# Optimization experiments

Measured on AMD Instinct MI355X. Metric: run time of the kernel, lower is better.

Reference implementation:

```python
import jax, jax.numpy as jnp
import numpy as np

TOPK_RATIOS = (0.67, 0.75, 0.8)


def setup_inputs() -> dict:
    key = jax.random.key(0)
    k0, k1, k2 = jax.random.split(key, 3)
    B, L, S, H, E, D = 4, 2048, 2048, 8, 64, 64
    queries = jax.random.normal(k0, (B, L, H, E), dtype=jnp.float32)
    keys = jax.random.normal(k1, (B, S, H, E), dtype=jnp.float32)
    values = jax.random.normal(k2, (B, S, H, D), dtype=jnp.float32)
    attn_weights = jnp.ones((len(TOPK_RATIOS),), dtype=jnp.float32)  # nn.Parameter(ones)
    attn_mask = jnp.zeros((1,), dtype=bool)  # unused by the module
    return {"queries": queries, "keys": keys, "values": values,
            "attn_weights": attn_weights, "attn_mask": attn_mask}


def reference(queries, keys, values, attn_weights, attn_mask):
    # queries: [B,L,H,E], keys: [B,S,H,E], values: [B,S,H,D]
    B, L, H, E = queries.shape
    S = keys.shape[1]
    scale = 1.0 / np.sqrt(E)  # self.scale is None -> 1/sqrt(E)
    scores = jnp.einsum('blhe,bshe->bhls', queries, keys) * scale  # [B,H,L,S]
    out = jnp.zeros(queries.shape[:3] + (values.shape[-1],), dtype=scores.dtype)
    for i, ratio in enumerate(TOPK_RATIOS):
        k = int(S * ratio)
        topv = jax.lax.top_k(scores, k)[0]            # sorted descending
        kth = topv[..., -1:]                           # k-th largest per row
        # mask==0 -> -inf, then softmax over S (ties at threshold are measure-zero)
        masked = jnp.where(scores >= kth, scores, -jnp.inf)
        attn = jax.nn.softmax(masked, axis=-1)         # dropout = identity (eval)
        out = out + jnp.einsum('bhls,bshd->blhd', attn, values) * attn_weights[i]
    return out
```

## Files before the change

kernel.cpp:

```cpp
#include <hip/hip_runtime.h>
#include <hip/hip_fp16.h>

typedef _Float16 f16x8 __attribute__((ext_vector_type(8)));
typedef float f32x4 __attribute__((ext_vector_type(4)));

#define KSEL0 1372u
#define KSEL1 1536u
#define KSEL2 1638u
#define WSC 16.0f
#define CSH 8.0f

__device__ __forceinline__ unsigned ou16_of(unsigned hb) {
  return hb ^ ((hb & 0x8000u) ? 0xFFFFu : 0x8000u);
}
__device__ __forceinline__ unsigned ou16_inv(unsigned ou) {
  return (ou & 0x8000u) ? (ou ^ 0x8000u) : (ou ^ 0xFFFFu);
}
__device__ __forceinline__ unsigned pk2(float a, float b) {
  auto h = __builtin_amdgcn_cvt_pkrtz(a, b);
  return __builtin_bit_cast(unsigned, h);
}
__device__ __forceinline__ unsigned shflx(unsigned v, int m) {
  return (unsigned)__shfl_xor((int)v, m, 64);
}
__device__ __forceinline__ float h2f(unsigned bits16) {
  return __half2float(__ushort_as_half((unsigned short)bits16));
}

__device__ __forceinline__ unsigned sel_digit_s(const unsigned* histw, unsigned k,
                                                int lane, int shift) {
  uint4 hr = ((const uint4*)histw)[lane];
  unsigned hx = (hr.x >> shift) & 0xFFFFu;
  unsigned hy = (hr.y >> shift) & 0xFFFFu;
  unsigned hz = (hr.z >> shift) & 0xFFFFu;
  unsigned hw_ = (hr.w >> shift) & 0xFFFFu;
  unsigned s4 = hx + hy + hz + hw_;
  unsigned p = s4;
  #pragma unroll
  for (int off = 1; off < 64; off <<= 1) {
    int sl = lane + off;
    unsigned t = (unsigned)__shfl((int)p, sl < 64 ? sl : lane, 64);
    p += (sl < 64) ? t : 0u;
  }
  unsigned a3 = p - s4;
  unsigned a2 = a3 + hw_;
  unsigned a1 = a2 + hz;
  unsigned a0 = a1 + hy;
  int d = -1; unsigned nk = 0;
  if (a3 < k && a3 + hw_ >= k)      { d = 4*lane+3; nk = k - a3; }
  else if (a2 < k && a2 + hz >= k)  { d = 4*lane+2; nk = k - a2; }
  else if (a1 < k && a1 + hy >= k)  { d = 4*lane+1; nk = k - a1; }
  else if (a0 < k && a0 + hx >= k)  { d = 4*lane+0; nk = k - a0; }
  unsigned long long mb = __ballot(d >= 0);
  int src = __ffsll(mb) - 1;
  unsigned pack = ((unsigned)d << 16) | nk;
  return (unsigned)__shfl((int)pack, src, 64);
}

extern "C" __global__ __launch_bounds__(256)
void prep_k(const float* __restrict__ K, unsigned short* __restrict__ Kh) {
  int idx = blockIdx.x * 256 + threadIdx.x;
  int ec = idx & 7;
  int s  = (idx >> 3) & 2047;
  int bh = idx >> 14;
  int b = bh >> 3, h = bh & 7;
  const float* src = K + (((size_t)b * 2048 + s) * 8 + h) * 64 + ec * 8;
  float4 a = *(const float4*)src;
  float4 c = *(const float4*)(src + 4);
  uint4 val = { pk2(a.x, a.y), pk2(a.z, a.w), pk2(c.x, c.y), pk2(c.z, c.w) };
  *(uint4*)(Kh + (size_t)idx * 8) = val;
}

extern "C" __global__ __launch_bounds__(256)
void prep_v(const float* __restrict__ V, unsigned short* __restrict__ Vt) {
  const int tid  = threadIdx.x;
  const int w    = tid >> 6;
  const int lane = tid & 63;
  const int u_   = lane >> 4;
  const int dq   = (lane >> 2) & 3;
  const int r_   = lane & 3;
  const unsigned selv = (lane & 1) ? 0x03020706u : 0x05040100u;

  int bh = blockIdx.x >> 4;
  int s0 = (blockIdx.x & 15) * 128;
  int b = bh >> 3, h = bh & 7;
  const float* Vb = V + ((size_t)b * 2048 * 8 + h) * 64;
  unsigned short* Vo = Vt + (size_t)bh * 64 * 2048;

  #pragma unroll
  for (int sp = 0; sp < 2; ++sp) {
    #pragma unroll
    for (int p = 0; p < 4; ++p) {
      int sl = w * 32 + sp * 16 + u_ * 4;
      int sg = s0 + sl + r_;
      int d0 = p * 16 + dq * 4;
      float4 f = *(const float4*)(Vb + (size_t)sg * 512 + d0);
      unsigned lo = pk2(f.x, f.y), hi = pk2(f.z, f.w);
      unsigned tlo = shflx(lo, 1), thi = shflx(hi, 1);
      lo = __builtin_amdgcn_perm(tlo, lo, selv);
      hi = __builtin_amdgcn_perm(thi, hi, selv);
      unsigned t2lo = shflx(lo, 2), t2hi = shflx(hi, 2);
      unsigned Aw = (lane & 2) ? t2hi : lo;
      unsigned Bw = (lane & 2) ? hi   : t2lo;
      int d = d0 + r_;
      uint2 wv = {Aw, Bw};
      *(uint2*)(Vo + (size_t)d * 2048 + s0 + sl) = wv;
    }
  }
}

extern "C" __global__ __launch_bounds__(512, 4)
void nma_kernel(const float* __restrict__ Q, const unsigned short* __restrict__ Kh,
                const unsigned short* __restrict__ Vt, const float* __restrict__ AW,
                float* __restrict__ Out)
{
  __shared__ __align__(16) char lds[81920];
  unsigned* work = (unsigned*)(lds + 65536);

  const int tid  = threadIdx.x;
  const int w    = tid >> 6;
  const int lane = tid & 63;
  const int g    = lane >> 4;
  const int lx   = lane & 15;

  int bid = blockIdx.x;
  int lb  = (bid & 7) * 512 + (bid >> 3);
  int bh  = lb >> 7;
  int b   = bh >> 3, hh = bh & 7;
  int l0  = (lb & 127) << 4;

  const float* Qb = Q + (((size_t)b * 2048 + l0) * 8 + hh) * 64;
  const unsigned short* Khb = Kh + (size_t)bh * 2048 * 64;
  const unsigned short* Vtb = Vt + (size_t)bh * 64 * 2048;

  {
    uint4 z4 = {0u,0u,0u,0u};
    uint4* p = (uint4*)work;
    p[tid] = z4;
    p[tid + 512] = z4;
  }

  union FU { f16x8 v; unsigned u[4]; };
  FU qa0, qa1;
  {
    const float* qp = Qb + (size_t)lx * 512 + g * 8;
    float4 a = *(const float4*)(qp);
    float4 c = *(const float4*)(qp + 4);
    qa0.u[0] = pk2(a.x*0.125f, a.y*0.125f); qa0.u[1] = pk2(a.z*0.125f, a.w*0.125f);
    qa0.u[2] = pk2(c.x*0.125f, c.y*0.125f); qa0.u[3] = pk2(c.z*0.125f, c.w*0.125f);
    a = *(const float4*)(qp + 32);
    c = *(const float4*)(qp + 36);
    qa1.u[0] = pk2(a.x*0.125f, a.y*0.125f); qa1.u[1] = pk2(a.z*0.125f, a.w*0.125f);
    qa1.u[2] = pk2(c.x*0.125f, c.y*0.125f); qa1.u[3] = pk2(c.z*0.125f, c.w*0.125f);
  }
  __syncthreads();

  const unsigned swl = ((unsigned)(lx & 7)) << 4;
  unsigned* hq = work + lx * 256;
  #pragma unroll 2
  for (int t = 0; t < 16; ++t) {
    int s0 = (t * 8 + w) * 16;
    const unsigned short* kp = Khb + (size_t)(s0 + lx) * 64 + g * 8;
    f16x8 kb0 = *(const f16x8*)(kp);
    f16x8 kb1 = *(const f16x8*)(kp + 32);
    f32x4 acc = {0.f, 0.f, 0.f, 0.f};
    acc = __builtin_amdgcn_mfma_f32_16x16x32_f16(kb0, qa0.v, acc, 0, 0, 0);
    acc = __builtin_amdgcn_mfma_f32_16x16x32_f16(kb1, qa1.v, acc, 0, 0, 0);
    unsigned u0 = pk2(acc[0], acc[1]);
    unsigned u1 = pk2(acc[2], acc[3]);
    uint2 wv = {u0, u1};
    *(uint2*)(lds + lx * 4096 + (((unsigned)(s0 * 2 + g * 8)) ^ swl)) = wv;
    atomicAdd(&hq[ou16_of(u0 & 0xFFFFu) >> 8], 1u);
    atomicAdd(&hq[ou16_of(u0 >> 16) >> 8], 1u);
    atomicAdd(&hq[ou16_of(u1 & 0xFFFFu) >> 8], 1u);
    atomicAdd(&hq[ou16_of(u1 >> 16) >> 8], 1u);
  }
  __syncthreads();

  const float aw0 = AW[0], aw1 = AW[1], aw2 = AW[2];

  unsigned d0a[2], d1a[2], d2a[2], k0a[2], k1a[2], k2a[2];
  #pragma unroll 2
  for (int rr = 0; rr < 2; ++rr) {
    int q = 2 * w + rr;
    const unsigned* hw1 = work + q * 256;
    unsigned p0 = sel_digit_s(hw1, KSEL0, lane, 0);
    unsigned p1 = sel_digit_s(hw1, KSEL1, lane, 0);
    unsigned p2 = sel_digit_s(hw1, KSEL2, lane, 0);
    d0a[rr] = p0 >> 16; k0a[rr] = p0 & 0xFFFFu;
    d1a[rr] = p1 >> 16; k1a[rr] = p1 & 0xFFFFu;
    d2a[rr] = p2 >> 16; k2a[rr] = p2 & 0xFFFFu;
  }

  unsigned* hw2 = work + w * 512;
  #pragma unroll 1
  for (int rr = 0; rr < 2; ++rr) {
    int q = 2 * w + rr;
    const unsigned swq = ((unsigned)(q & 7)) << 4;
    char* rowp = lds + q * 4096;
    for (int i = lane; i < 512; i += 64) hw2[i] = 0u;
    unsigned D0 = d0a[rr], D1 = d1a[rr], D2 = d2a[rr];

    unsigned ereg[16];
    #pragma unroll
    for (int it = 0; it < 4; ++it) {
      uint4 dv = *(const uint4*)(rowp + (((unsigned)(it * 1024 + lane * 16)) ^ swq));
      unsigned ws[4] = {dv.x, dv.y, dv.z, dv.w};
      #pragma unroll
      for (int p = 0; p < 4; ++p) {
        unsigned b0 = ws[p] & 0xFFFFu, b1 = ws[p] >> 16;
        unsigned o0 = ou16_of(b0), o1 = ou16_of(b1);
        unsigned hi0 = o0 >> 8, lo0 = o0 & 255u;
        unsigned hi1 = o1 >> 8, lo1 = o1 & 255u;
        unsigned add0 = (hi0 == D0 ? 1u : 0u) | (hi0 == D1 ? 0x10000u : 0u);
        unsigned add1 = (hi1 == D0 ? 1u : 0u) | (hi1 == D1 ? 0x10000u : 0u);
        if (add0) atomicAdd(&hw2[lo0], add0);
        if (hi0 == D2) atomicAdd(&hw2[256 + lo0], 1u);
        if (add1) atomicAdd(&hw2[lo1], add1);
        if (hi1 == D2) atomicAdd(&hw2[256 + lo1], 1u);
        float e0 = __expf(h2f(b0) - CSH);
        float e1 = __expf(h2f(b1) - CSH);
        ereg[it * 4 + p] = pk2(e0, e1);
      }
    }
    unsigned T1o = (D0 << 8) | (sel_digit_s(hw2,       k0a[rr], lane, 0)  >> 16);
    unsigned T2o = (D1 << 8) | (sel_digit_s(hw2,       k1a[rr], lane, 16) >> 16);
    unsigned T3o = (D2 << 8) | (sel_digit_s(hw2 + 256, k2a[rr], lane, 0)  >> 16);
    unsigned e1b = pk2(__expf(h2f(ou16_inv(T1o)) - CSH), 0.f) & 0xFFFFu;
    unsigned e2b = pk2(__expf(h2f(ou16_inv(T2o)) - CSH), 0.f) & 0xFFFFu;
    unsigned e3b = pk2(__expf(h2f(ou16_inv(T3o)) - CSH), 0.f) & 0xFFFFu;

    float zbA = 0.f, zbB = 0.f, zbC = 0.f;
    #pragma unroll
    for (int i = 0; i < 16; ++i) {
      unsigned uu = ereg[i];
      unsigned b0 = uu & 0xFFFFu, b1 = uu >> 16;
      float e0 = h2f(b0), e1 = h2f(b1);
      if (b0 >= e1b) zbA += e0; else if (b0 >= e2b) zbB += e0; else if (b0 >= e3b) zbC += e0;
      if (b1 >= e1b) zbA += e1; else if (b1 >= e2b) zbB += e1; else if (b1 >= e3b) zbC += e1;
    }
    #pragma unroll
    for (int off = 1; off < 64; off <<= 1) {
      zbA += __shfl_xor(zbA, off, 64);
      zbB += __shfl_xor(zbB, off, 64);
      zbC += __shfl_xor(zbC, off, 64);
    }
    float z1 = zbA, z2 = zbA + zbB, z3 = z2 + zbC;
    float A3 = aw2 / z3;
    float A2 = aw1 / z2 + A3;
    float A1 = aw0 / z1 + A2;
    unsigned A1b = pk2(A1 * WSC, 0.f) & 0xFFFFu;
    unsigned A2b = pk2(A2 * WSC, 0.f) & 0xFFFFu;
    unsigned A3b = pk2(A3 * WSC, 0.f) & 0xFFFFu;

    #pragma unroll
    for (int it = 0; it < 4; ++it) {
      unsigned no[4];
      #pragma unroll
      for (int p = 0; p < 4; ++p) {
        unsigned uu = ereg[it * 4 + p];
        unsigned b0 = uu & 0xFFFFu, b1 = uu >> 16;
        unsigned c0 = (b0 >= e1b) ? A1b : (b0 >= e2b) ? A2b : (b0 >= e3b) ? A3b : 0u;
        unsigned c1 = (b1 >= e1b) ? A1b : (b1 >= e2b) ? A2b : (b1 >= e3b) ? A3b : 0u;
        unsigned cw = c0 | (c1 << 16);
        __half2 prod = *(__half2*)&uu * *(__half2*)&cw;
        no[p] = *(unsigned*)&prod;
      }
      uint4 nv = {no[0], no[1], no[2], no[3]};
      *(uint4*)(rowp + (((unsigned)(it * 1024 + lane * 16)) ^ swq)) = nv;
    }
  }
  __syncthreads();

  f32x4 oacc = {0.f, 0.f, 0.f, 0.f};
  const int dt = (w >> 1) * 16;
  const int sh = w & 1;
  const unsigned short* vp = Vtb + (size_t)(dt + lx) * 2048 + sh * 1024 + g * 8;
  const char* bp = lds + lx * 4096;

  #pragma unroll 8
  for (int kc = 0; kc < 32; ++kc) {
    f16x8 av = *(const f16x8*)(vp + kc * 32);
    unsigned sb = (unsigned)((sh * 1024 + kc * 32 + g * 8) * 2);
    f16x8 bv = *(const f16x8*)(bp + (sb ^ swl));
    oacc = __builtin_amdgcn_mfma_f32_16x16x32_f16(av, bv, oacc, 0, 0, 0);
  }

  float* pbuf = (float*)work;
  *(f32x4*)(pbuf + w * 256 + lx * 16 + g * 4) = oacc;
  __syncthreads();
  if (w < 4) {
    const float* pa = pbuf + (2 * w) * 256 + lx * 16 + g * 4;
    float4 ra = *(const float4*)pa;
    float4 rb = *(const float4*)(pa + 256);
    float* op = Out + (((size_t)b * 2048 + l0 + lx) * 8 + hh) * 64 + w * 16 + g * 4;
    float4 ov = { (ra.x + rb.x) * (1.f/WSC), (ra.y + rb.y) * (1.f/WSC),
                  (ra.z + rb.z) * (1.f/WSC), (ra.w + rb.w) * (1.f/WSC) };
    *(float4*)op = ov;
  }
}

extern "C" void kernel_launch(void* const* d_in, const int* in_sizes, int n_in,
                              void* d_out, int out_size, void* d_ws, size_t ws_size,
                              hipStream_t stream) {
  (void)in_sizes; (void)n_in; (void)out_size; (void)ws_size;
  const float* Q  = (const float*)d_in[0];
  const float* K  = (const float*)d_in[1];
  const float* V  = (const float*)d_in[2];
  const float* AW = (const float*)d_in[3];
  unsigned short* Kh = (unsigned short*)d_ws;
  unsigned short* Vt = (unsigned short*)((char*)d_ws + 8388608);
  prep_k<<<dim3(2048), dim3(256), 0, stream>>>(K, Kh);
  prep_v<<<dim3(512),  dim3(256), 0, stream>>>(V, Vt);
  nma_kernel<<<dim3(4096), dim3(512), 0, stream>>>(Q, Kh, Vt, AW, (float*)d_out);
}
```

Before: 375.0 us.

## Merge prep kernels, rotate histogram bins, share prefix scans, prefetch V before barrier

Merges the K and V conversion kernels into one launch to save a kernel launch. Rotates each row's histogram bins by a per-row offset to spread LDS atomic bank conflicts, then unrotates the read by indexing with (lane+q)&63. Computes the 64-lane suffix scan once per histogram and shares it across the three threshold picks instead of rescanning each time. Prefetches the first V fragments before the final barrier and raises unroll factors. The rotation makes correctness depend on the unrotate indexing matching exactly.

```diff
diff --git a/kernel.cpp b/kernel.cpp
--- a/kernel.cpp
+++ b/kernel.cpp
@@ -27,14 +27,7 @@
   return __half2float(__ushort_as_half((unsigned short)bits16));
 }
 
-__device__ __forceinline__ unsigned sel_digit_s(const unsigned* histw, unsigned k,
-                                                int lane, int shift) {
-  uint4 hr = ((const uint4*)histw)[lane];
-  unsigned hx = (hr.x >> shift) & 0xFFFFu;
-  unsigned hy = (hr.y >> shift) & 0xFFFFu;
-  unsigned hz = (hr.z >> shift) & 0xFFFFu;
-  unsigned hw_ = (hr.w >> shift) & 0xFFFFu;
-  unsigned s4 = hx + hy + hz + hw_;
+__device__ __forceinline__ unsigned suffix64(unsigned s4, int lane) {
   unsigned p = s4;
   #pragma unroll
   for (int off = 1; off < 64; off <<= 1) {
@@ -42,7 +35,12 @@
     unsigned t = (unsigned)__shfl((int)p, sl < 64 ? sl : lane, 64);
     p += (sl < 64) ? t : 0u;
   }
-  unsigned a3 = p - s4;
+  return p;
+}
+__device__ __forceinline__ unsigned pick_digit(unsigned tail, unsigned hx, unsigned hy,
+                                               unsigned hz, unsigned hw_, unsigned k, int lane) {
+  unsigned s4 = hx + hy + hz + hw_;
+  unsigned a3 = tail - s4;
   unsigned a2 = a3 + hw_;
   unsigned a1 = a2 + hz;
   unsigned a0 = a1 + hy;
@@ -58,53 +56,54 @@
 }
 
 extern "C" __global__ __launch_bounds__(256)
-void prep_k(const float* __restrict__ K, unsigned short* __restrict__ Kh) {
-  int idx = blockIdx.x * 256 + threadIdx.x;
-  int ec = idx & 7;
-  int s  = (idx >> 3) & 2047;
-  int bh = idx >> 14;
-  int b = bh >> 3, h = bh & 7;
-  const float* src = K + (((size_t)b * 2048 + s) * 8 + h) * 64 + ec * 8;
-  float4 a = *(const float4*)src;
-  float4 c = *(const float4*)(src + 4);
-  uint4 val = { pk2(a.x, a.y), pk2(a.z, a.w), pk2(c.x, c.y), pk2(c.z, c.w) };
-  *(uint4*)(Kh + (size_t)idx * 8) = val;
-}
-
-extern "C" __global__ __launch_bounds__(256)
-void prep_v(const float* __restrict__ V, unsigned short* __restrict__ Vt) {
-  const int tid  = threadIdx.x;
-  const int w    = tid >> 6;
-  const int lane = tid & 63;
-  const int u_   = lane >> 4;
-  const int dq   = (lane >> 2) & 3;
-  const int r_   = lane & 3;
-  const unsigned selv = (lane & 1) ? 0x03020706u : 0x05040100u;
-
-  int bh = blockIdx.x >> 4;
-  int s0 = (blockIdx.x & 15) * 128;
-  int b = bh >> 3, h = bh & 7;
-  const float* Vb = V + ((size_t)b * 2048 * 8 + h) * 64;
-  unsigned short* Vo = Vt + (size_t)bh * 64 * 2048;
-
-  #pragma unroll
-  for (int sp = 0; sp < 2; ++sp) {
-    #pragma unroll
-    for (int p = 0; p < 4; ++p) {
-      int sl = w * 32 + sp * 16 + u_ * 4;
-      int sg = s0 + sl + r_;
-      int d0 = p * 16 + dq * 4;
-      float4 f = *(const float4*)(Vb + (size_t)sg * 512 + d0);
-      unsigned lo = pk2(f.x, f.y), hi = pk2(f.z, f.w);
-      unsigned tlo = shflx(lo, 1), thi = shflx(hi, 1);
-      lo = __builtin_amdgcn_perm(tlo, lo, selv);
-      hi = __builtin_amdgcn_perm(thi, hi, selv);
-      unsigned t2lo = shflx(lo, 2), t2hi = shflx(hi, 2);
-      unsigned Aw = (lane & 2) ? t2hi : lo;
-      unsigned Bw = (lane & 2) ? hi   : t2lo;
-      int d = d0 + r_;
-      uint2 wv = {Aw, Bw};
-      *(uint2*)(Vo + (size_t)d * 2048 + s0 + sl) = wv;
+void prep_kv(const float* __restrict__ K, const float* __restrict__ V,
+             unsigned short* __restrict__ Kh, unsigned short* __restrict__ Vt) {
+  if (blockIdx.x < 2048) {
+    int idx = blockIdx.x * 256 + threadIdx.x;
+    int ec = idx & 7;
+    int s  = (idx >> 3) & 2047;
+    int bh = idx >> 14;
+    int b = bh >> 3, h = bh & 7;
+    const float* src = K + (((size_t)b * 2048 + s) * 8 + h) * 64 + ec * 8;
+    float4 a = *(const float4*)src;
+    float4 c = *(const float4*)(src + 4);
+    uint4 val = { pk2(a.x, a.y), pk2(a.z, a.w), pk2(c.x, c.y), pk2(c.z, c.w) };
+    *(uint4*)(Kh + (size_t)idx * 8) = val;
+  } else {
+    const int bid  = blockIdx.x - 2048;
+    const int tid  = threadIdx.x;
+    const int w    = tid >> 6;
+    const int lane = tid & 63;
+    const int u_   = lane >> 4;
+    const int dq   = (lane >> 2) & 3;
+    const int r_   = lane & 3;
+    const unsigned selv = (lane & 1) ? 0x03020706u : 0x05040100u;
+
+    int bh = bid >> 4;
+    int s0 = (bid & 15) * 128;
+    int b = bh >> 3, h = bh & 7;
+    const float* Vb = V + ((size_t)b * 2048 * 8 + h) * 64;
+    unsigned short* Vo = Vt + (size_t)bh * 64 * 2048;
+
+    #pragma unroll
+    for (int sp = 0; sp < 2; ++sp) {
+      #pragma unroll
+      for (int p = 0; p < 4; ++p) {
+        int sl = w * 32 + sp * 16 + u_ * 4;
+        int sg = s0 + sl + r_;
+        int d0 = p * 16 + dq * 4;
+        float4 f = *(const float4*)(Vb + (size_t)sg * 512 + d0);
+        unsigned lo = pk2(f.x, f.y), hi = pk2(f.z, f.w);
+        unsigned tlo = shflx(lo, 1), thi = shflx(hi, 1);
+        lo = __builtin_amdgcn_perm(tlo, lo, selv);
+        hi = __builtin_amdgcn_perm(thi, hi, selv);
+        unsigned t2lo = shflx(lo, 2), t2hi = shflx(hi, 2);
+        unsigned Aw = (lane & 2) ? t2hi : lo;
+        unsigned Bw = (lane & 2) ? hi   : t2lo;
+        int d = d0 + r_;
+        uint2 wv = {Aw, Bw};
+        *(uint2*)(Vo + (size_t)d * 2048 + s0 + sl) = wv;
+      }
     }
   }
 }
@@ -156,8 +155,9 @@
   __syncthreads();
 
   const unsigned swl = ((unsigned)(lx & 7)) << 4;
+  const unsigned rot = ((unsigned)lx) << 2;
   unsigned* hq = work + lx * 256;
-  #pragma unroll 2
+  #pragma unroll 4
   for (int t = 0; t < 16; ++t) {
     int s0 = (t * 8 + w) * 16;
     const unsigned short* kp = Khb + (size_t)(s0 + lx) * 64 + g * 8;
@@ -170,10 +170,10 @@
     unsigned u1 = pk2(acc[2], acc[3]);
     uint2 wv = {u0, u1};
     *(uint2*)(lds + lx * 4096 + (((unsigned)(s0 * 2 + g * 8)) ^ swl)) = wv;
-    atomicAdd(&hq[ou16_of(u0 & 0xFFFFu) >> 8], 1u);
-    atomicAdd(&hq[ou16_of(u0 >> 16) >> 8], 1u);
-    atomicAdd(&hq[ou16_of(u1 & 0xFFFFu) >> 8], 1u);
-    atomicAdd(&hq[ou16_of(u1 >> 16) >> 8], 1u);
+    atomicAdd(&hq[((ou16_of(u0 & 0xFFFFu) >> 8) + rot) & 255u], 1u);
+    atomicAdd(&hq[((ou16_of(u0 >> 16) >> 8) + rot) & 255u], 1u);
+    atomicAdd(&hq[((ou16_of(u1 & 0xFFFFu) >> 8) + rot) & 255u], 1u);
+    atomicAdd(&hq[((ou16_of(u1 >> 16) >> 8) + rot) & 255u], 1u);
   }
   __syncthreads();
 
@@ -183,10 +183,11 @@
   #pragma unroll 2
   for (int rr = 0; rr < 2; ++rr) {
     int q = 2 * w + rr;
-    const unsigned* hw1 = work + q * 256;
-    unsigned p0 = sel_digit_s(hw1, KSEL0, lane, 0);
-    unsigned p1 = sel_digit_s(hw1, KSEL1, lane, 0);
-    unsigned p2 = sel_digit_s(hw1, KSEL2, lane, 0);
+    uint4 hb = ((const uint4*)(work + q * 256))[(lane + q) & 63];
+    unsigned tail = suffix64(hb.x + hb.y + hb.z + hb.w, lane);
+    unsigned p0 = pick_digit(tail, hb.x, hb.y, hb.z, hb.w, KSEL0, lane);
+    unsigned p1 = pick_digit(tail, hb.x, hb.y, hb.z, hb.w, KSEL1, lane);
+    unsigned p2 = pick_digit(tail, hb.x, hb.y, hb.z, hb.w, KSEL2, lane);
     d0a[rr] = p0 >> 16; k0a[rr] = p0 & 0xFFFFu;
     d1a[rr] = p1 >> 16; k1a[rr] = p1 & 0xFFFFu;
     d2a[rr] = p2 >> 16; k2a[rr] = p2 & 0xFFFFu;
@@ -223,9 +224,16 @@
         ereg[it * 4 + p] = pk2(e0, e1);
       }
     }
-    unsigned T1o = (D0 << 8) | (sel_digit_s(hw2,       k0a[rr], lane, 0)  >> 16);
-    unsigned T2o = (D1 << 8) | (sel_digit_s(hw2,       k1a[rr], lane, 16) >> 16);
-    unsigned T3o = (D2 << 8) | (sel_digit_s(hw2 + 256, k2a[rr], lane, 0)  >> 16);
+    uint4 pkv = ((const uint4*)hw2)[lane];
+    uint4 d2v = ((const uint4*)(hw2 + 256))[lane];
+    unsigned hx = pkv.x & 0xFFFFu, hy = pkv.y & 0xFFFFu, hz = pkv.z & 0xFFFFu, hw_ = pkv.w & 0xFFFFu;
+    unsigned t0 = suffix64(hx + hy + hz + hw_, lane);
+    unsigned T1o = (D0 << 8) | (pick_digit(t0, hx, hy, hz, hw_, k0a[rr], lane) >> 16);
+    hx = pkv.x >> 16; hy = pkv.y >> 16; hz = pkv.z >> 16; hw_ = pkv.w >> 16;
+    unsigned t1 = suffix64(hx + hy + hz + hw_, lane);
+    unsigned T2o = (D1 << 8) | (pick_digit(t1, hx, hy, hz, hw_, k1a[rr], lane) >> 16);
+    unsigned t2 = suffix64(d2v.x + d2v.y + d2v.z + d2v.w, lane);
+    unsigned T3o = (D2 << 8) | (pick_digit(t2, d2v.x, d2v.y, d2v.z, d2v.w, k2a[rr], lane) >> 16);
     unsigned e1b = pk2(__expf(h2f(ou16_inv(T1o)) - CSH), 0.f) & 0xFFFFu;
     unsigned e2b = pk2(__expf(h2f(ou16_inv(T2o)) - CSH), 0.f) & 0xFFFFu;
     unsigned e3b = pk2(__expf(h2f(ou16_inv(T3o)) - CSH), 0.f) & 0xFFFFu;
@@ -270,19 +278,33 @@
       *(uint4*)(rowp + (((unsigned)(it * 1024 + lane * 16)) ^ swq)) = nv;
     }
   }
-  __syncthreads();
-
-  f32x4 oacc = {0.f, 0.f, 0.f, 0.f};
+
   const int dt = (w >> 1) * 16;
   const int sh = w & 1;
   const unsigned short* vp = Vtb + (size_t)(dt + lx) * 2048 + sh * 1024 + g * 8;
+  f16x8 pv0 = *(const f16x8*)(vp);
+  f16x8 pv1 = *(const f16x8*)(vp + 32);
+  f16x8 pv2 = *(const f16x8*)(vp + 64);
+  f16x8 pv3 = *(const f16x8*)(vp + 96);
+  __syncthreads();
+
+  f32x4 oacc = {0.f, 0.f, 0.f, 0.f};
   const char* bp = lds + lx * 4096;
-
-  #pragma unroll 8
-  for (int kc = 0; kc < 32; ++kc) {
+  const unsigned sbase = (unsigned)((sh * 1024 + g * 8) * 2);
+
+  oacc = __builtin_amdgcn_mfma_f32_16x16x32_f16(pv0,
+           *(const f16x8*)(bp + ((sbase +   0u) ^ swl)), oacc, 0, 0, 0);
+  oacc = __builtin_amdgcn_mfma_f32_16x16x32_f16(pv1,
+           *(const f16x8*)(bp + ((sbase +  64u) ^ swl)), oacc, 0, 0, 0);
+  oacc = __builtin_amdgcn_mfma_f32_16x16x32_f16(pv2,
+           *(const f16x8*)(bp + ((sbase + 128u) ^ swl)), oacc, 0, 0, 0);
+  oacc = __builtin_amdgcn_mfma_f32_16x16x32_f16(pv3,
+           *(const f16x8*)(bp + ((sbase + 192u) ^ swl)), oacc, 0, 0, 0);
+
+  #pragma unroll 4
+  for (int kc = 4; kc < 32; ++kc) {
     f16x8 av = *(const f16x8*)(vp + kc * 32);
-    unsigned sb = (unsigned)((sh * 1024 + kc * 32 + g * 8) * 2);
-    f16x8 bv = *(const f16x8*)(bp + (sb ^ swl));
+    f16x8 bv = *(const f16x8*)(bp + ((sbase + (unsigned)(kc * 64)) ^ swl));
     oacc = __builtin_amdgcn_mfma_f32_16x16x32_f16(av, bv, oacc, 0, 0, 0);
   }
 
@@ -310,7 +332,6 @@
   const float* AW = (const float*)d_in[3];
   unsigned short* Kh = (unsigned short*)d_ws;
   unsigned short* Vt = (unsigned short*)((char*)d_ws + 8388608);
-  prep_k<<<dim3(2048), dim3(256), 0, stream>>>(K, Kh);
-  prep_v<<<dim3(512),  dim3(256), 0, stream>>>(V, Vt);
+  prep_kv<<<dim3(2560), dim3(256), 0, stream>>>(K, V, Kh, Vt);
   nma_kernel<<<dim3(4096), dim3(512), 0, stream>>>(Q, Kh, Vt, AW, (float*)d_out);
 }
```

Measured after the change: 352.4 us. 6.0% less time.
